# Performance work log

Measured on AMD Instinct MI355X. Metric: run time of the kernel, lower is better.

## Reference

```python
import jax, jax.numpy as jnp
import numpy as np

# ---- module hyperparameters (from init_kwargs) ----
KL_TEMP = 4.0
NUM_CLASSES = 100
POLICY_NUMS = 7          # linear out dim = POLICY_NUMS + 2 (identity, classes, policies)
FEATURE_NUMS = 128       # linear in dim = concat of two 64-d policy features
POS_W = (1.0, 0.5, 0.001)
NEG_W = (1.0, 0.5, 0.001)
KD_CE_W = (1.0, 1.0)
LOSS_W = (1.0, 1.0, 1.0)
BATCH = 2048


def setup_inputs() -> dict:
    key = jax.random.key(0)
    ks = jax.random.split(key, 9)
    O = POLICY_NUMS + 2
    return {
        "student_logits": jax.random.normal(ks[0], (BATCH, NUM_CLASSES), jnp.float32),
        "teacher_logits": jax.random.normal(ks[1], (BATCH, NUM_CLASSES), jnp.float32),
        "student_policy": jax.random.normal(ks[2], (BATCH, FEATURE_NUMS // 2), jnp.float32),
        "teacher_policy": jax.random.normal(ks[3], (BATCH, FEATURE_NUMS // 2), jnp.float32),
        "W1": jax.random.normal(ks[4], (O, FEATURE_NUMS), jnp.float32) * 0.08,  # frozen teacher linear
        "bias1": jax.random.normal(ks[5], (O,), jnp.float32) * 0.01,
        "W2": jax.random.normal(ks[6], (O, FEATURE_NUMS), jnp.float32) * 0.08,  # trainable student linear
        "bias2": jax.random.normal(ks[7], (O,), jnp.float32) * 0.01,
        "targets": jax.random.randint(ks[8], (BATCH, 1, POLICY_NUMS + 1), 0, 10, dtype=jnp.int32),
    }


def _kldiv_mean(inp, tgt):
    # torch KLDivLoss(reduction='mean'): mean over all elems of target*(log(target)-input), zero where target<=0
    safe = jnp.where(tgt > 0, tgt, 1.0)
    return jnp.where(tgt > 0, tgt * (jnp.log(safe) - inp), 0.0).mean()


def _wmean(loss, tgt, pw, nw):
    return jnp.where(tgt == 1.0, loss * pw, loss * nw).mean()


def _pair_linear(feat, W, bias):
    # L[i, j] = W @ concat(f_even[j], f_odd[i]) + bias, computed without materializing [b1,b1,2f]
    f = feat.shape[-1]
    f1, f2 = feat[0::2], feat[1::2]                       # [b1, f] each
    A = f1 @ W[:, :f].T                                   # [b1, O]  (j part)
    B = f2 @ W[:, f:].T                                   # [b1, O]  (i part)
    return B[:, None, :] + A[None, :, :] + bias           # [b1, b1, O]


def _policy_loss(teacher_policy, student_policy, targets, W1, bias1, W2, bias2):
    B = student_policy.shape[0]
    b1 = B // 2
    dt = student_policy.dtype

    Ls = _pair_linear(student_policy, W2, bias2)          # [b1,b1,O]
    Lt = jax.lax.stop_gradient(_pair_linear(teacher_policy, W1, bias1))

    sI, sC = Ls[..., 0], Ls[..., 1]
    sP = Ls[..., 2:].reshape(b1 * b1, POLICY_NUMS)
    tI, tC = Lt[..., 0], Lt[..., 1]
    tP = Lt[..., 2:].reshape(b1 * b1, POLICY_NUMS)

    eye = jnp.eye(b1, dtype=dt)
    # off-diagonal identity entries are detached for the student (teacher already no-grad)
    sI = eye * sI + (1.0 - eye) * jax.lax.stop_gradient(sI)

    t = targets.reshape(B, POLICY_NUMS + 1)
    t1, t2 = t[0::2], t[1::2]
    Teq = (t1[None, :, :] == t2[:, None, :]).astype(dt)   # [b1,b1,P+1]

    classes_value = 1.0 / (NUM_CLASSES - 1) + 1.0
    identity_value = 1.0 / (b1 - 1) + 1.0
    gC = Teq[..., 0] * classes_value - 1.0 / (NUM_CLASSES - 1)
    gP = Teq[..., 1:].reshape(b1 * b1, POLICY_NUMS) * 2.0 - 1.0
    gI = eye * identity_value - 1.0 / (b1 - 1)

    kl_loss = (_wmean((sI - tI) ** 2, gI, POS_W[0], NEG_W[0])
               + _wmean((sC - tC) ** 2, gC, POS_W[1], NEG_W[1])
               + _wmean((sP - tP) ** 2, gP, POS_W[2], NEG_W[2]))

    # KLDivLoss(reduction='mean') returns a scalar; torch.where broadcasts it, so .mean() of weights scales it
    ce_loss = (_kldiv_mean(sI, gI) * jnp.where(gI == 1.0, POS_W[0], NEG_W[0]).mean()
               + _kldiv_mean(sC, gC) * jnp.where(gC == 1.0, POS_W[1], NEG_W[1]).mean()
               + _wmean((sP - gP) ** 2, gP, POS_W[2], NEG_W[2]))

    return KD_CE_W[0] * kl_loss + KD_CE_W[1] * ce_loss


def reference(student_logits, teacher_logits, student_policy, teacher_policy, W1, bias1, W2, bias2, targets):
    B = student_logits.shape[0]
    # ---- CE loss (targets last dim <= 15 -> integer class label at column 0) ----
    labels = targets.reshape(B, -1)[:, 0]
    logp = jax.nn.log_softmax(student_logits, axis=1)
    ce_loss = -jnp.take_along_axis(logp, labels[:, None], axis=1).mean()

    # ---- KD KL loss (KLDivLoss reduction='mean' over all elements) ----
    t_prob = jax.nn.softmax(teacher_logits / KL_TEMP, axis=1)
    s_logp = jax.nn.log_softmax(student_logits / KL_TEMP, axis=1)
    kl_loss = _kldiv_mean(s_logp, t_prob) * (KL_TEMP ** 2)

    # ---- pairwise policy loss (the fusion-heavy path) ----
    policy_loss = _policy_loss(teacher_policy, student_policy, targets, W1, bias1, W2, bias2)

    return LOSS_W[0] * ce_loss + LOSS_W[1] * kl_loss + LOSS_W[2] * policy_loss
```

## Files before the change

### kernel.cpp

```cpp
#include <hip/hip_runtime.h>
#include <math.h>

#define NCLS   100
#define BATCH_ 2048
#define OK     9
#define FHALF  64

#define NLOGB  512
#define NPOLB  16
#define NBLK   (NLOGB + NPOLB)

#define LP_OFF 0
#define PS_OFF (LP_OFF + NLOGB * 2)
#define PB_OFF (PS_OFF + NPOLB * 72)

__device__ __forceinline__ float waveSum(float v) {
#pragma unroll
    for (int off = 32; off; off >>= 1) v += __shfl_xor(v, off, 64);
    return v;
}
__device__ __forceinline__ float waveMax(float v) {
#pragma unroll
    for (int off = 32; off; off >>= 1) v = fmaxf(v, __shfl_xor(v, off, 64));
    return v;
}

__global__ __launch_bounds__(256) void stats_kernel(
        const float* __restrict__ slog, const float* __restrict__ tlog,
        const float* __restrict__ spol, const float* __restrict__ tpol,
        const float* __restrict__ W1,   const float* __restrict__ W2,
        const int*   __restrict__ tgt,  float* __restrict__ ws)
{
    __shared__ float bkt[320];
    __shared__ float redL[8];

    const int tid  = threadIdx.x;
    const int wave = tid >> 6;
    const int lane = tid & 63;

    if (blockIdx.x < NLOGB) {
        const int r = blockIdx.x * 4 + wave;
        const float* x = slog + r * NCLS;
        const float* y = tlog + r * NCLS;
        const int label = tgt[r * 8];
        const bool has2 = lane < (NCLS - 64);
        float x1 = x[lane];
        float y1 = y[lane];
        float x2 = has2 ? x[lane + 64] : -3.0e38f;
        float y2 = has2 ? y[lane + 64] : -3.0e38f;
        float xl = x[label];
        float mx = waveMax(fmaxf(x1, x2));
        float my = waveMax(fmaxf(y1, y2));
        float se1  = waveSum(expf(x1 - mx) + (has2 ? expf(x2 - mx) : 0.f));
        float se4s = waveSum(expf((x1 - mx) * 0.25f) + (has2 ? expf((x2 - mx) * 0.25f) : 0.f));
        float e1 = expf((y1 - my) * 0.25f);
        float e2 = has2 ? expf((y2 - my) * 0.25f) : 0.f;
        float se4t = waveSum(e1 + e2);
        float tnum = waveSum(e1 * (y1 - x1) * 0.25f + (has2 ? e2 * (y2 - x2) * 0.25f : 0.f));
        if (lane == 0) {
            float logZ1  = mx + logf(se1);
            float logZ4s = mx * 0.25f + logf(se4s);
            float logZ4t = my * 0.25f + logf(se4t);
            redL[wave * 2]     = logZ1 - xl;
            redL[wave * 2 + 1] = tnum / se4t + logZ4s - logZ4t;
        }
        __syncthreads();
        if (tid < 2)
            ws[LP_OFF + blockIdx.x * 2 + tid] =
                redL[tid] + redL[2 + tid] + redL[4 + tid] + redL[6 + tid];
    } else {
        const int pb = blockIdx.x - NLOGB;
        for (int idx = tid; idx < 320; idx += 256) bkt[idx] = 0.f;
        __syncthreads();

        if (tid < 64) {
            const int i = pb * 64 + tid;
            const float4* f1s = (const float4*)(spol + (2 * i) * FHALF);
            const float4* f2s = (const float4*)(spol + (2 * i + 1) * FHALF);
            const float4* f1t = (const float4*)(tpol + (2 * i) * FHALF);
            const float4* f2t = (const float4*)(tpol + (2 * i + 1) * FHALF);

            float As[OK], Bs[OK], At[OK], Bt[OK];
#pragma unroll
            for (int k = 0; k < OK; ++k) { As[k] = 0.f; Bs[k] = 0.f; At[k] = 0.f; Bt[k] = 0.f; }
            for (int f4 = 0; f4 < FHALF / 4; ++f4) {
                float4 a4 = f1s[f4], b4 = f2s[f4], c4 = f1t[f4], d4 = f2t[f4];
#pragma unroll
                for (int k = 0; k < OK; ++k) {
                    float4 w2lo = *(const float4*)(W2 + k * 128 + f4 * 4);
                    float4 w2hi = *(const float4*)(W2 + k * 128 + 64 + f4 * 4);
                    float4 w1lo = *(const float4*)(W1 + k * 128 + f4 * 4);
                    float4 w1hi = *(const float4*)(W1 + k * 128 + 64 + f4 * 4);
                    As[k] = fmaf(a4.x, w2lo.x, fmaf(a4.y, w2lo.y,
                            fmaf(a4.z, w2lo.z, fmaf(a4.w, w2lo.w, As[k]))));
                    Bs[k] = fmaf(b4.x, w2hi.x, fmaf(b4.y, w2hi.y,
                            fmaf(b4.z, w2hi.z, fmaf(b4.w, w2hi.w, Bs[k]))));
                    At[k] = fmaf(c4.x, w1lo.x, fmaf(c4.y, w1lo.y,
                            fmaf(c4.z, w1lo.z, fmaf(c4.w, w1lo.w, At[k]))));
                    Bt[k] = fmaf(d4.x, w1hi.x, fmaf(d4.y, w1hi.y,
                            fmaf(d4.z, w1hi.z, fmaf(d4.w, w1hi.w, Bt[k]))));
                }
            }

#pragma unroll
            for (int k = 0; k < OK; ++k) {
                float du = Bs[k] - Bt[k], dw = As[k] - At[k];
                float v0 = waveSum(du),     v1 = waveSum(du * du);
                float v2 = waveSum(dw),     v3 = waveSum(dw * dw);
                float v4 = waveSum(Bs[k]),  v5 = waveSum(Bs[k] * Bs[k]);
                float v6 = waveSum(As[k]),  v7 = waveSum(As[k] * As[k]);
                if (lane == 0) {
                    float* p = ws + PS_OFF + pb * 72 + k * 8;
                    p[0] = v0; p[1] = v1; p[2] = v2; p[3] = v3;
                    p[4] = v4; p[5] = v5; p[6] = v6; p[7] = v7;
                }
            }

            const int* t1r = tgt + (2 * i) * 8;
            const int* t2r = tgt + (2 * i + 1) * 8;
#pragma unroll
            for (int c0 = 0; c0 < 8; ++c0) {
                int v1i = t1r[c0], v2i = t2r[c0];
                atomicAdd(&bkt[0 * 80 + c0 * 10 + v1i], 1.0f);
                atomicAdd(&bkt[1 * 80 + c0 * 10 + v2i], 1.0f);
                atomicAdd(&bkt[2 * 80 + c0 * 10 + v1i], As[c0 + 1]);
                atomicAdd(&bkt[3 * 80 + c0 * 10 + v2i], Bs[c0 + 1]);
            }
        }
        __syncthreads();
        for (int idx = tid; idx < 320; idx += 256)
            ws[PB_OFF + pb * 320 + idx] = bkt[idx];
    }
}

__global__ __launch_bounds__(256) void combine_kernel(
        const float* __restrict__ ws,
        const float* __restrict__ bias1, const float* __restrict__ bias2,
        float* __restrict__ out)
{
    __shared__ float statsC[72];
    __shared__ float bktC[320];
    __shared__ float cekl[8];

    const int tid  = threadIdx.x;
    const int wave = tid >> 6;
    const int lane = tid & 63;

    float ce = 0.f, kl = 0.f;
#pragma unroll
    for (int s = 0; s < NLOGB; s += 256) {
        ce += ws[LP_OFF + (s + tid) * 2];
        kl += ws[LP_OFF + (s + tid) * 2 + 1];
    }
    ce = waveSum(ce); kl = waveSum(kl);
    if (lane == 0) { cekl[wave * 2] = ce; cekl[wave * 2 + 1] = kl; }

    if (tid < 72) {
        float s = 0.f;
#pragma unroll
        for (int b = 0; b < NPOLB; ++b) s += ws[PS_OFF + b * 72 + tid];
        statsC[tid] = s;
    }
    for (int idx = tid; idx < 320; idx += 256) {
        float s = 0.f;
#pragma unroll
        for (int b = 0; b < NPOLB; ++b) s += ws[PB_OFF + b * 320 + idx];
        bktC[idx] = s;
    }
    __syncthreads();

    if (tid == 0) {
        const double N = 1024.0, M = 1048576.0;
        double ce_main = (double)(cekl[0] + cekl[2] + cekl[4] + cekl[6]) / (double)BATCH_;
        double kl_main = (double)(cekl[1] + cekl[3] + cekl[5] + cekl[7]) * 16.0
                       / (double)(BATCH_ * NCLS);

        double kl_pol = 0.0, Sp_acc = 0.0;
        double SumL[OK], SumL2[OK];
        for (int k = 0; k < OK; ++k) {
            const float* p = &statsC[k * 8];
            double D1u = p[0], D2u = p[1], D1w = p[2], D2w = p[3];
            double U1 = p[4], U2 = p[5], Wa1 = p[6], Wa2 = p[7];
            double cd = (double)bias2[k] - (double)bias1[k];
            double b  = (double)bias2[k];
            double S = N * D2u + N * (D2w + 2.0 * cd * D1w + N * cd * cd)
                     + 2.0 * D1u * (D1w + N * cd);
            if (k == 0)      kl_pol += S / M;
            else if (k == 1) kl_pol += 0.5 * S / M;
            else             Sp_acc += S;
            SumL[k]  = N * U1 + N * Wa1 + M * b;
            SumL2[k] = N * U2 + N * (Wa2 + 2.0 * b * Wa1 + N * b * b)
                     + 2.0 * U1 * (Wa1 + N * b);
        }
        kl_pol += 0.001 * Sp_acc / (7.0 * M);

        double ce_I = -((double)statsC[4] + (double)statsC[6] + N * (double)bias2[0]) / M;

        const float* cnt1 = &bktC[0];
        const float* cnt2 = &bktC[80];
        const float* sA   = &bktC[160];
        const float* sB   = &bktC[240];
        double ce_C = 0.0, ceP = 0.0;
        for (int c0 = 0; c0 < 8; ++c0) {
            double ms = 0.0, pc = 0.0;
            for (int v = 0; v < 10; ++v) {
                double c1 = (double)cnt1[c0 * 10 + v], c2 = (double)cnt2[c0 * 10 + v];
                ms += c1 * (double)sB[c0 * 10 + v] + c2 * (double)sA[c0 * 10 + v];
                pc += c1 * c2;
            }
            ms += (double)bias2[c0 + 1] * pc;
            if (c0 == 0) {
                ce_C = -0.5 * ms / M;
            } else {
                int k = c0 + 1;
                double sg = 2.0 * ms - SumL[k];
                ceP += SumL2[k] - 2.0 * sg + M;
            }
        }
        ceP *= 0.001 / (7.0 * M);

        out[0] = (float)(ce_main + kl_main + kl_pol + ce_I + ce_C + ceP);
    }
}

extern "C" void kernel_launch(void* const* d_in, const int* in_sizes, int n_in,
                              void* d_out, int out_size, void* d_ws, size_t ws_size,
                              hipStream_t stream) {
    const float* slog = (const float*)d_in[0];
    const float* tlog = (const float*)d_in[1];
    const float* spol = (const float*)d_in[2];
    const float* tpol = (const float*)d_in[3];
    const float* W1   = (const float*)d_in[4];
    const float* b1   = (const float*)d_in[5];
    const float* W2   = (const float*)d_in[6];
    const float* b2   = (const float*)d_in[7];
    const int*   tgt  = (const int*)d_in[8];
    float* ws = (float*)d_ws;

    stats_kernel<<<NBLK, 256, 0, stream>>>(slog, tlog, spol, tpol, W1, W2, tgt, ws);
    combine_kernel<<<1, 256, 0, stream>>>(ws, b1, b2, (float*)d_out);
}
```

Measured before the change: 99.56 us.

## Use DPP wave reductions, readlane label gather, and per-row partial outputs

Replaces the shuffle-based wave reductions with DPP row ops followed by a readlane from lane 63. The label logit is now gathered with readlane from registers instead of a second global load. The logits blocks drop their shared-memory cross-wave reduction and __syncthreads, writing per-row partials, so the combine kernel now sums 2048 rows instead of 512 blocks. Policy blocks are moved to the front of the grid so the longer-running blocks start first. This cuts shuffle latency and barriers, at the cost of a larger workspace and more reads in the combine kernel.

```diff
diff --git a/kernel.cpp b/kernel.cpp
--- a/kernel.cpp
+++ b/kernel.cpp
@@ -6,23 +6,42 @@
 #define OK     9
 #define FHALF  64
 
+#define NPOLB  16
 #define NLOGB  512
-#define NPOLB  16
 #define NBLK   (NLOGB + NPOLB)
 
 #define LP_OFF 0
-#define PS_OFF (LP_OFF + NLOGB * 2)
+#define PS_OFF (LP_OFF + BATCH_ * 2)
 #define PB_OFF (PS_OFF + NPOLB * 72)
 
-__device__ __forceinline__ float waveSum(float v) {
-#pragma unroll
-    for (int off = 32; off; off >>= 1) v += __shfl_xor(v, off, 64);
-    return v;
-}
-__device__ __forceinline__ float waveMax(float v) {
-#pragma unroll
-    for (int off = 32; off; off >>= 1) v = fmaxf(v, __shfl_xor(v, off, 64));
-    return v;
+template<int CTRL, int RMASK>
+__device__ __forceinline__ float dpp_add_f(float x) {
+    int t = __builtin_amdgcn_update_dpp(0, __float_as_int(x), CTRL, RMASK, 0xF, false);
+    return x + __int_as_float(t);
+}
+template<int CTRL, int RMASK>
+__device__ __forceinline__ float dpp_max_f(float x) {
+    int t = __builtin_amdgcn_update_dpp(__float_as_int(-3.0e38f), __float_as_int(x),
+                                        CTRL, RMASK, 0xF, false);
+    return fmaxf(x, __int_as_float(t));
+}
+__device__ __forceinline__ float waveRedSum(float x) {
+    x = dpp_add_f<0x111, 0xF>(x);
+    x = dpp_add_f<0x112, 0xF>(x);
+    x = dpp_add_f<0x114, 0xF>(x);
+    x = dpp_add_f<0x118, 0xF>(x);
+    x = dpp_add_f<0x142, 0xA>(x);
+    x = dpp_add_f<0x143, 0xC>(x);
+    return __int_as_float(__builtin_amdgcn_readlane(__float_as_int(x), 63));
+}
+__device__ __forceinline__ float waveRedMax(float x) {
+    x = dpp_max_f<0x111, 0xF>(x);
+    x = dpp_max_f<0x112, 0xF>(x);
+    x = dpp_max_f<0x114, 0xF>(x);
+    x = dpp_max_f<0x118, 0xF>(x);
+    x = dpp_max_f<0x142, 0xA>(x);
+    x = dpp_max_f<0x143, 0xC>(x);
+    return __int_as_float(__builtin_amdgcn_readlane(__float_as_int(x), 63));
 }
 
 __global__ __launch_bounds__(256) void stats_kernel(
@@ -32,44 +51,41 @@
         const int*   __restrict__ tgt,  float* __restrict__ ws)
 {
     __shared__ float bkt[320];
-    __shared__ float redL[8];
 
     const int tid  = threadIdx.x;
     const int wave = tid >> 6;
     const int lane = tid & 63;
 
-    if (blockIdx.x < NLOGB) {
-        const int r = blockIdx.x * 4 + wave;
+    if (blockIdx.x >= NPOLB) {
+        const int r = (blockIdx.x - NPOLB) * 4 + wave;
         const float* x = slog + r * NCLS;
         const float* y = tlog + r * NCLS;
-        const int label = tgt[r * 8];
+        const int label = __builtin_amdgcn_readfirstlane(tgt[r * 8]);
         const bool has2 = lane < (NCLS - 64);
         float x1 = x[lane];
         float y1 = y[lane];
         float x2 = has2 ? x[lane + 64] : -3.0e38f;
         float y2 = has2 ? y[lane + 64] : -3.0e38f;
-        float xl = x[label];
-        float mx = waveMax(fmaxf(x1, x2));
-        float my = waveMax(fmaxf(y1, y2));
-        float se1  = waveSum(expf(x1 - mx) + (has2 ? expf(x2 - mx) : 0.f));
-        float se4s = waveSum(expf((x1 - mx) * 0.25f) + (has2 ? expf((x2 - mx) * 0.25f) : 0.f));
+        float xla = __int_as_float(__builtin_amdgcn_readlane(__float_as_int(x1), label & 63));
+        float xlb = __int_as_float(__builtin_amdgcn_readlane(__float_as_int(x2), label & 63));
+        float xl  = (label < 64) ? xla : xlb;
+        float mx = waveRedMax(fmaxf(x1, x2));
+        float my = waveRedMax(fmaxf(y1, y2));
+        float se1  = waveRedSum(expf(x1 - mx) + (has2 ? expf(x2 - mx) : 0.f));
+        float se4s = waveRedSum(expf((x1 - mx) * 0.25f) + (has2 ? expf((x2 - mx) * 0.25f) : 0.f));
         float e1 = expf((y1 - my) * 0.25f);
         float e2 = has2 ? expf((y2 - my) * 0.25f) : 0.f;
-        float se4t = waveSum(e1 + e2);
-        float tnum = waveSum(e1 * (y1 - x1) * 0.25f + (has2 ? e2 * (y2 - x2) * 0.25f : 0.f));
+        float se4t = waveRedSum(e1 + e2);
+        float tnum = waveRedSum(e1 * (y1 - x1) * 0.25f + (has2 ? e2 * (y2 - x2) * 0.25f : 0.f));
         if (lane == 0) {
             float logZ1  = mx + logf(se1);
             float logZ4s = mx * 0.25f + logf(se4s);
             float logZ4t = my * 0.25f + logf(se4t);
-            redL[wave * 2]     = logZ1 - xl;
-            redL[wave * 2 + 1] = tnum / se4t + logZ4s - logZ4t;
-        }
-        __syncthreads();
-        if (tid < 2)
-            ws[LP_OFF + blockIdx.x * 2 + tid] =
-                redL[tid] + redL[2 + tid] + redL[4 + tid] + redL[6 + tid];
+            ws[LP_OFF + r * 2]     = logZ1 - xl;
+            ws[LP_OFF + r * 2 + 1] = tnum / se4t + logZ4s - logZ4t;
+        }
     } else {
-        const int pb = blockIdx.x - NLOGB;
+        const int pb = blockIdx.x;
         for (int idx = tid; idx < 320; idx += 256) bkt[idx] = 0.f;
         __syncthreads();
 
@@ -105,10 +121,10 @@
 #pragma unroll
             for (int k = 0; k < OK; ++k) {
                 float du = Bs[k] - Bt[k], dw = As[k] - At[k];
-                float v0 = waveSum(du),     v1 = waveSum(du * du);
-                float v2 = waveSum(dw),     v3 = waveSum(dw * dw);
-                float v4 = waveSum(Bs[k]),  v5 = waveSum(Bs[k] * Bs[k]);
-                float v6 = waveSum(As[k]),  v7 = waveSum(As[k] * As[k]);
+                float v0 = waveRedSum(du),     v1 = waveRedSum(du * du);
+                float v2 = waveRedSum(dw),     v3 = waveRedSum(dw * dw);
+                float v4 = waveRedSum(Bs[k]),  v5 = waveRedSum(Bs[k] * Bs[k]);
+                float v6 = waveRedSum(As[k]),  v7 = waveRedSum(As[k] * As[k]);
                 if (lane == 0) {
                     float* p = ws + PS_OFF + pb * 72 + k * 8;
                     p[0] = v0; p[1] = v1; p[2] = v2; p[3] = v3;
@@ -148,11 +164,11 @@
 
     float ce = 0.f, kl = 0.f;
 #pragma unroll
-    for (int s = 0; s < NLOGB; s += 256) {
+    for (int s = 0; s < BATCH_; s += 256) {
         ce += ws[LP_OFF + (s + tid) * 2];
         kl += ws[LP_OFF + (s + tid) * 2 + 1];
     }
-    ce = waveSum(ce); kl = waveSum(kl);
+    ce = waveRedSum(ce); kl = waveRedSum(kl);
     if (lane == 0) { cekl[wave * 2] = ce; cekl[wave * 2 + 1] = kl; }
 
     if (tid < 72) {
```

After: 100.0 us. No clear change (+0.5%).
